# Performance work log

Measured on AMD Instinct MI355X. Metric: run time of the kernel, lower is better.

## Reference

```python
import jax, jax.numpy as jnp
import numpy as np

N_NODES = 50000
N_EDGES = 600000
IN_DIM = 128
HID_DIM = 128


def setup_inputs() -> dict:
    key = jax.random.key(0)
    ks = jax.random.split(key, 6)
    x = jax.random.normal(ks[0], (N_NODES, IN_DIM), dtype=jnp.float32)
    edge_index = jax.random.randint(ks[1], (2, N_EDGES), 0, N_NODES, dtype=jnp.int32)
    # GCNConv linear weights (applied as x @ W) and biases
    W1 = jax.random.normal(ks[2], (IN_DIM, HID_DIM), dtype=jnp.float32) * (1.0 / np.sqrt(IN_DIM))
    b1 = jnp.zeros((HID_DIM,), dtype=jnp.float32)
    W2 = jax.random.normal(ks[3], (HID_DIM, HID_DIM), dtype=jnp.float32) * (1.0 / np.sqrt(HID_DIM))
    b2 = jnp.zeros((HID_DIM,), dtype=jnp.float32)
    return {"x": x, "edge_index": edge_index, "W1": W1, "b1": b1, "W2": W2, "b2": b2}


def _gcn_norm(edge_index, num_nodes):
    # add self-loops (edge_weight=None -> all ones), symmetric normalization
    loop = jnp.arange(num_nodes, dtype=edge_index.dtype)
    src = jnp.concatenate([edge_index[0], loop])  # [E+N]
    dst = jnp.concatenate([edge_index[1], loop])  # [E+N]
    ew = jnp.ones(src.shape[0], dtype=jnp.float32)
    deg = jax.ops.segment_sum(ew, dst, num_segments=num_nodes)  # in-degree incl. self-loop
    dinv = jnp.where(deg > 0, jax.lax.rsqrt(deg), 0.0)
    norm = dinv[src] * ew * dinv[dst]  # [E+N]
    return src, dst, norm


def _gcn_layer(z, W, b, src, dst, norm, num_nodes):
    h = z @ W  # [N, H] dense transform
    msg = h[src] * norm[:, None]  # gather + scale  [E+N, H]
    agg = jax.ops.segment_sum(msg, dst, num_segments=num_nodes)  # scatter-add [N, H]
    return agg + b


def reference(x, edge_index, W1, b1, W2, b2):
    num_nodes = x.shape[0]
    src, dst, norm = _gcn_norm(edge_index, num_nodes)
    z = jax.nn.relu(_gcn_layer(x, W1, b1, src, dst, norm, num_nodes))
    z = jax.nn.relu(_gcn_layer(z, W2, b2, src, dst, norm, num_nodes))
    return z
```

## Files before the change

### kernel.cpp

```cpp
#include <hip/hip_runtime.h>

#define NN 50000
#define NE 600000
#define DIM 128
#define CAP 40

#define OFF_CUR    0
#define OFF_DINV   200704
#define OFF_FLAG   401408
#define OFF_SRCL   401920
#define OFF_W1T    8401920
#define OFF_W2T    8434688
#define OFF_Y      8467456
#define OFF_Z1     21267456

typedef unsigned short u16;
typedef unsigned int u32;
typedef __attribute__((ext_vector_type(8))) short short8;
typedef __attribute__((ext_vector_type(4))) float floatx4;

__device__ __forceinline__ float bflo(u32 u) { return __uint_as_float(u << 16); }
__device__ __forceinline__ float bfhi(u32 u) { return __uint_as_float(u & 0xFFFF0000u); }
__device__ __forceinline__ u16 f2bf(float f) {
    u32 x = __float_as_uint(f);
    return (u16)((x + 0x7FFFu + ((x >> 16) & 1u)) >> 16);
}
__device__ __forceinline__ u32 pack2(float hi, float lo) {
    return ((u32)f2bf(hi) << 16) | (u32)f2bf(lo);
}

__global__ __launch_bounds__(256) void k_init(
    const int* __restrict__ ei, const float* __restrict__ W1,
    const float* __restrict__ W2, char* __restrict__ ws) {
    int* cur = (int*)(ws + OFF_CUR);
    int* flagw = (int*)(ws + OFF_FLAG);
    u16* W1t = (u16*)(ws + OFF_W1T);
    u16* W2t = (u16*)(ws + OFF_W2T);
    int b = blockIdx.x, tid = threadIdx.x;
    for (int i = b * 256 + tid; i < NN; i += 128 * 256) cur[i] = 0;
    const float* W = (b < 64) ? W1 : W2;
    u16* Wt = (b < 64) ? W1t : W2t;
    int e = (b & 63) * 256 + tid;
    int k = e >> 7, n = e & 127;
    Wt[n * DIM + k] = f2bf(W[e]);
    if (b == 0) {
        __shared__ int sc;
        if (tid == 0) sc = 0;
        __syncthreads();
        int lc = 0;
        for (int i = tid; i < 4096; i += 256) lc += (ei[2 * i + 1] != 0) ? 1 : 0;
        if (lc) atomicAdd(&sc, lc);
        __syncthreads();
        if (tid == 0) *flagw = (sc < 64) ? 1 : 0;
    }
}

__global__ __launch_bounds__(256) void k_fill(const int* __restrict__ ei,
                                              char* __restrict__ ws) {
    int* cur = (int*)(ws + OFF_CUR);
    int* srclist = (int*)(ws + OFF_SRCL);
    int is64 = *(const int*)(ws + OFF_FLAG);
    int i = blockIdx.x * 256 + threadIdx.x;
    if (i >= NE) return;
    int d = is64 ? ei[2 * (NE + i)] : ei[NE + i];
    if ((u32)d >= NN) return;
    int p = atomicAdd(&cur[d], 1);
    if (p < CAP) {
        int s = is64 ? ei[2 * i] : ei[i];
        srclist[d * CAP + p] = ((u32)s < NN) ? s : 0;
    }
}

__global__ __launch_bounds__(256) void k_scale(const float* __restrict__ x,
                                               char* __restrict__ ws) {
    const int* cur = (const int*)(ws + OFF_CUR);
    float* dinv = (float*)(ws + OFF_DINV);
    u32* y = (u32*)(ws + OFF_Y);
    int i = blockIdx.x * 256 + threadIdx.x;
    if (i >= NN * 64) return;
    int n = i >> 6;
    float dn = rsqrtf((float)(cur[n] + 1));
    if ((i & 63) == 0) dinv[n] = dn;
    float2 v = ((const float2*)x)[i];
    y[i] = pack2(dn * v.y, dn * v.x);
}

__global__ __launch_bounds__(256) void k_layer(
    const u32* __restrict__ y, const char* __restrict__ ws,
    const u16* __restrict__ Bt, const float* __restrict__ bias,
    void* __restrict__ out, int mode) {
    const int* cur = (const int*)(ws + OFF_CUR);
    const int* srclist = (const int*)(ws + OFF_SRCL);
    const float* dinv = (const float*)(ws + OFF_DINV);
    __shared__ u32 tl[16][68];
    int tid = threadIdx.x;
    int wv = tid >> 6, lane = tid & 63;
    int node0 = blockIdx.x << 4;

    for (int q = 0; q < 4; ++q) {
        int n = node0 + wv * 4 + q;
        int cnt = cur[n];
        cnt = cnt < CAP ? cnt : CAP;
        float dn = dinv[n];
        const int* sl = srclist + (size_t)n * CAP;
        u32 us = y[(size_t)n * 64 + lane];
        float a0 = bflo(us), a1 = bfhi(us);
        if (cnt) {
            int c1 = cnt - 1;
#define IDX(j) sl[(((j) < c1) ? (j) : c1)]
            u32 u0 = y[(size_t)IDX(0) * 64 + lane];
            u32 u1 = y[(size_t)IDX(1) * 64 + lane];
            u32 u2 = y[(size_t)IDX(2) * 64 + lane];
            u32 u3 = y[(size_t)IDX(3) * 64 + lane];
            int sN = IDX(4);
#pragma unroll 2
            for (int i = 0; i < cnt; ++i) {
                int sNN = IDX(i + 5);
                u32 u4 = y[(size_t)sN * 64 + lane];
                a0 += bflo(u0); a1 += bfhi(u0);
                u0 = u1; u1 = u2; u2 = u3; u3 = u4;
                sN = sNN;
            }
#undef IDX
        }
        tl[wv * 4 + q][lane] = pack2(dn * a1, dn * a0);
    }
    __syncthreads();

    int m = lane & 15, kg = lane >> 4;
    floatx4 acc[2];
    acc[0] = (floatx4){0.f, 0.f, 0.f, 0.f};
    acc[1] = (floatx4){0.f, 0.f, 0.f, 0.f};
#pragma unroll
    for (int kk = 0; kk < 4; ++kk) {
        int k0 = kk * 32 + kg * 8;
        short8 a = *(const short8*)&tl[m][kk * 16 + kg * 4];
#pragma unroll
        for (int j = 0; j < 2; ++j) {
            int nt = wv * 2 + j;
            short8 b = *(const short8*)(Bt + (size_t)(nt * 16 + m) * DIM + k0);
            acc[j] = __builtin_amdgcn_mfma_f32_16x16x32_bf16(a, b, acc[j], 0, 0, 0);
        }
    }
    float4 d4 = (mode == 0) ? *(const float4*)(dinv + node0 + kg * 4)
                            : make_float4(1.f, 1.f, 1.f, 1.f);
#pragma unroll
    for (int j = 0; j < 2; ++j) {
        int col = (wv * 2 + j) * 16 + m;
        float bv = bias[col];
#pragma unroll
        for (int r = 0; r < 4; ++r) {
            int row = node0 + kg * 4 + r;
            float v = acc[j][r] + bv;
            v = v > 0.f ? v : 0.f;
            if (mode == 0)
                ((u16*)out)[(size_t)row * DIM + col] = f2bf(v * (&d4.x)[r]);
            else
                ((float*)out)[(size_t)row * DIM + col] = v;
        }
    }
}

extern "C" void kernel_launch(void* const* d_in, const int* in_sizes, int n_in,
                              void* d_out, int out_size, void* d_ws, size_t ws_size,
                              hipStream_t stream) {
    (void)in_sizes; (void)n_in; (void)out_size; (void)ws_size;
    const float* x  = (const float*)d_in[0];
    const int*   ei = (const int*)d_in[1];
    const float* W1 = (const float*)d_in[2];
    const float* b1 = (const float*)d_in[3];
    const float* W2 = (const float*)d_in[4];
    const float* b2 = (const float*)d_in[5];
    char* ws = (char*)d_ws;

    u16* W1t = (u16*)(ws + OFF_W1T);
    u16* W2t = (u16*)(ws + OFF_W2T);
    u32* y   = (u32*)(ws + OFF_Y);
    u32* z1  = (u32*)(ws + OFF_Z1);

    k_init<<<128, 256, 0, stream>>>(ei, W1, W2, ws);
    k_fill<<<(NE + 255) / 256, 256, 0, stream>>>(ei, ws);
    k_scale<<<(NN * 64 + 255) / 256, 256, 0, stream>>>(x, ws);
    k_layer<<<NN / 16, 256, 0, stream>>>(y, ws, W1t, b1, z1, 0);
    k_layer<<<NN / 16, 256, 0, stream>>>(z1, ws, W2t, b2, d_out, 1);
}
```

Baseline: 237.8 us.

## Aggregate four nodes per wavefront with 16-byte row gathers

The neighbour aggregation now gives each 16-lane group of a wavefront its own node, so one wave processes four nodes at once instead of looping over them one by one. Each lane loads a uint4 (8 bf16 values) per neighbour row instead of a single u32. Groups with fewer neighbours run to the wave-wide maximum degree, with masked and clamped indices. This adds memory-level parallelism and cuts the number of gather instructions, at the cost of idle iterations for low-degree nodes and more registers.

```diff
diff --git a/kernel.cpp b/kernel.cpp
--- a/kernel.cpp
+++ b/kernel.cpp
@@ -95,36 +95,55 @@
     __shared__ u32 tl[16][68];
     int tid = threadIdx.x;
     int wv = tid >> 6, lane = tid & 63;
+    int grp = lane >> 4, sl16 = lane & 15;
     int node0 = blockIdx.x << 4;
-
-    for (int q = 0; q < 4; ++q) {
-        int n = node0 + wv * 4 + q;
-        int cnt = cur[n];
-        cnt = cnt < CAP ? cnt : CAP;
-        float dn = dinv[n];
-        const int* sl = srclist + (size_t)n * CAP;
-        u32 us = y[(size_t)n * 64 + lane];
-        float a0 = bflo(us), a1 = bfhi(us);
-        if (cnt) {
-            int c1 = cnt - 1;
-#define IDX(j) sl[(((j) < c1) ? (j) : c1)]
-            u32 u0 = y[(size_t)IDX(0) * 64 + lane];
-            u32 u1 = y[(size_t)IDX(1) * 64 + lane];
-            u32 u2 = y[(size_t)IDX(2) * 64 + lane];
-            u32 u3 = y[(size_t)IDX(3) * 64 + lane];
-            int sN = IDX(4);
+    int nn = wv * 4 + grp;
+    int n = node0 + nn;
+    int cnt = cur[n];
+    cnt = cnt < CAP ? cnt : CAP;
+    float dn = dinv[n];
+    const int* sl = srclist + (size_t)n * CAP;
+    int c1 = cnt > 0 ? cnt - 1 : 0;
+
+    uint4 us = *(const uint4*)(y + (size_t)n * 64 + sl16 * 4);
+    float a0 = bflo(us.x), a1 = bfhi(us.x), a2 = bflo(us.y), a3 = bfhi(us.y);
+    float a4 = bflo(us.z), a5 = bfhi(us.z), a6 = bflo(us.w), a7 = bfhi(us.w);
+
+    int mx = cnt;
+    mx = max(mx, __shfl_xor(mx, 16));
+    mx = max(mx, __shfl_xor(mx, 32));
+
+#define SIDX(j) ((j) < cnt ? sl[(j) < c1 ? (j) : c1] : n)
+#define ROW(s) (*(const uint4*)(y + (size_t)(s) * 64 + sl16 * 4))
+#define MSK(j) (((j) < cnt) ? 0xFFFFFFFFu : 0u)
+    if (mx > 0) {
+        int s0 = SIDX(0), s1 = SIDX(1), s2 = SIDX(2), s3 = SIDX(3);
+        u32 m0 = MSK(0), m1 = MSK(1), m2 = MSK(2), m3 = MSK(3);
+        uint4 u0 = ROW(s0), u1 = ROW(s1), u2 = ROW(s2);
+        int sF = s3;
 #pragma unroll 2
-            for (int i = 0; i < cnt; ++i) {
-                int sNN = IDX(i + 5);
-                u32 u4 = y[(size_t)sN * 64 + lane];
-                a0 += bflo(u0); a1 += bfhi(u0);
-                u0 = u1; u1 = u2; u2 = u3; u3 = u4;
-                sN = sNN;
-            }
-#undef IDX
+        for (int i = 0; i < mx; ++i) {
+            int sN = SIDX(i + 4);
+            uint4 u3 = ROW(sF);
+            u32 v;
+            v = u0.x & m0; a0 += bflo(v); a1 += bfhi(v);
+            v = u0.y & m0; a2 += bflo(v); a3 += bfhi(v);
+            v = u0.z & m0; a4 += bflo(v); a5 += bfhi(v);
+            v = u0.w & m0; a6 += bflo(v); a7 += bfhi(v);
+            u0 = u1; u1 = u2; u2 = u3;
+            m0 = m1; m1 = m2; m2 = m3; m3 = MSK(i + 4);
+            sF = sN;
         }
-        tl[wv * 4 + q][lane] = pack2(dn * a1, dn * a0);
-    }
+    }
+#undef SIDX
+#undef ROW
+#undef MSK
+    uint4 o;
+    o.x = pack2(dn * a1, dn * a0);
+    o.y = pack2(dn * a3, dn * a2);
+    o.z = pack2(dn * a5, dn * a4);
+    o.w = pack2(dn * a7, dn * a6);
+    *(uint4*)&tl[nn][sl16 * 4] = o;
     __syncthreads();
 
     int m = lane & 15, kg = lane >> 4;
```

Result: faster. 195.9 us (-17.6%).
